# Optimization experiments

Measured on AMD Instinct MI355X. Metric: run time of the kernel, lower is better.

Reference implementation:

```python
import jax, jax.numpy as jnp
import numpy as np

B, S, D, H = 4, 2048, 1024, 16
HS = D // H  # head_size = 64


def setup_inputs() -> dict:
    key = jax.random.key(0)
    ks = jax.random.split(key, 6)
    scale = 0.02
    return {
        "token_embeddings": jax.random.normal(ks[0], (B, S, D), dtype=jnp.float32),
        # per-head projection weights, stacked: [H, D, HS] (x @ W per head)
        "Wq": jax.random.normal(ks[1], (H, D, HS), dtype=jnp.float32) * scale,
        "Wk": jax.random.normal(ks[2], (H, D, HS), dtype=jnp.float32) * scale,
        "Wv": jax.random.normal(ks[3], (H, D, HS), dtype=jnp.float32) * scale,
        # output projection (Linear with bias): y = x @ Wo + bo
        "Wo": jax.random.normal(ks[4], (D, D), dtype=jnp.float32) * scale,
        "bo": jax.random.normal(ks[5], (D,), dtype=jnp.float32) * scale,
    }


def reference(token_embeddings, Wq, Wk, Wv, Wo, bo):
    # Per-head projections, batched over heads: [B,H,S,HS]
    q = jnp.einsum("bsd,hde->bhse", token_embeddings, Wq)
    k = jnp.einsum("bsd,hde->bhse", token_embeddings, Wk)
    v = jnp.einsum("bsd,hde->bhse", token_embeddings, Wv)
    scale = HS ** -0.5
    scores = jnp.einsum("bhqe,bhke->bhqk", q, k) * scale  # [B,H,S,S]
    causal = jnp.tril(jnp.ones((S, S), dtype=bool))
    scores = jnp.where(causal, scores, -jnp.inf)
    weights = jax.nn.softmax(scores, axis=-1)
    # dropout in eval mode -> identity
    out = jnp.einsum("bhqk,bhke->bhqe", weights, v)  # [B,H,S,HS]
    # concat heads -> [B,S,D] (head order matches torch.cat over heads)
    out = out.transpose(0, 2, 1, 3).reshape(B, S, D)
    return out @ Wo + bo
```

## Files before the change

kernel.cpp:

```cpp
#include <hip/hip_runtime.h>


typedef __bf16 bf16;
typedef bf16 bf16x8 __attribute__((ext_vector_type(8)));
typedef bf16 bf16x4 __attribute__((ext_vector_type(4)));
typedef float f32x4 __attribute__((ext_vector_type(4)));

__device__ __forceinline__ void gload16(const void* gsrc, void* ldst) {
  __builtin_amdgcn_global_load_lds(
      (const __attribute__((address_space(1))) unsigned int*)gsrc,
      (__attribute__((address_space(3))) unsigned int*)ldst, 16, 0, 0);
}

__device__ __forceinline__ f32x4 mfma16(bf16x8 a, bf16x8 b, f32x4 c) {
  return __builtin_amdgcn_mfma_f32_16x16x32_bf16(a, b, c, 0, 0, 0);
}

__global__ __launch_bounds__(256) void pack_x_kernel(const float* __restrict__ x,
                                                     bf16* __restrict__ xb) {
  int i = (blockIdx.x * 256 + threadIdx.x) * 4;
  float4 v = *(const float4*)(x + i);
  bf16x4 o;
  o[0] = (bf16)v.x; o[1] = (bf16)v.y; o[2] = (bf16)v.z; o[3] = (bf16)v.w;
  *(bf16x4*)(xb + i) = o;
}

__global__ __launch_bounds__(256) void pack_wqkv_kernel(const float* __restrict__ Wq,
                                                        const float* __restrict__ Wk,
                                                        const float* __restrict__ Wv,
                                                        bf16* __restrict__ WT) {
  int idx = blockIdx.x * 256 + threadIdx.x;
  int n = idx >> 10, k = idx & 1023;
  int sel = n >> 10, nn = n & 1023;
  const float* W = (sel == 0) ? Wq : (sel == 1 ? Wk : Wv);
  int h = nn >> 6, e = nn & 63;
  WT[(size_t)n * 1024 + k] = (bf16)W[h * 65536 + k * 64 + e];
}

__global__ __launch_bounds__(256) void pack_wo_kernel(const float* __restrict__ Wo,
                                                      bf16* __restrict__ WoT) {
  int idx = blockIdx.x * 256 + threadIdx.x;
  int n = idx >> 10, k = idx & 1023;
  WoT[idx] = (bf16)Wo[k * 1024 + n];
}

template <bool F32OUT>
__global__ __launch_bounds__(256, 2) void gemm4_kernel(const bf16* __restrict__ A,
                                                       const bf16* __restrict__ BT,
                                                       bf16* __restrict__ Cb,
                                                       float* __restrict__ Cf,
                                                       const float* __restrict__ bias,
                                                       int N, int K) {
  __shared__ bf16 As[2][128 * 64];
  __shared__ bf16 Bs[2][128 * 64];
  const int tid = threadIdx.x, lane = tid & 63, wave = tid >> 6;
  const int g = lane >> 4, c = lane & 15;
  const int wr = wave >> 1, wc = wave & 1;
  const int bid = blockIdx.x;
  const int xcd = bid & 7, local = bid >> 3;
  const int m0 = (xcd * 8 + (local & 7)) * 128;
  const int n0 = (local >> 3) * 128;

  const int schunk = (lane & 7) ^ (lane >> 3);

#define STAGE4(T, S)                                                      \
  do {                                                                    \
    _Pragma("unroll") for (int j = 0; j < 4; ++j) {                       \
      const int r = wave * 32 + j * 8 + (lane >> 3);                      \
      const int ldso = wave * 4096 + j * 1024 + lane * 16;                \
      gload16(A + (size_t)(m0 + r) * K + (T)*64 + schunk * 8,             \
              (char*)&As[S][0] + ldso);                                   \
      gload16(BT + (size_t)(n0 + r) * K + (T)*64 + schunk * 8,            \
              (char*)&Bs[S][0] + ldso);                                   \
    }                                                                     \
  } while (0)

  f32x4 acc[4][4] = {};
  const int nt = K >> 6;
  STAGE4(0, 0);
  asm volatile("s_waitcnt vmcnt(0)" ::: "memory");
  __builtin_amdgcn_sched_barrier(0);
  __builtin_amdgcn_s_barrier();
  __builtin_amdgcn_sched_barrier(0);

#pragma unroll 1
  for (int t = 0; t < nt; ++t) {
    const int s = t & 1;
    if (t + 1 < nt) STAGE4(t + 1, s ^ 1);
    bf16x8 af[4][2], bfr[4][2];
#pragma unroll
    for (int m = 0; m < 4; ++m) {
      const int row = wr * 64 + m * 16 + c;
#pragma unroll
      for (int kk = 0; kk < 2; ++kk)
        af[m][kk] = *(const bf16x8*)((const char*)&As[s][0] + row * 128 +
                                     (((kk * 4 + g) ^ (row & 7)) << 4));
    }
#pragma unroll
    for (int n = 0; n < 4; ++n) {
      const int row = wc * 64 + n * 16 + c;
#pragma unroll
      for (int kk = 0; kk < 2; ++kk)
        bfr[n][kk] = *(const bf16x8*)((const char*)&Bs[s][0] + row * 128 +
                                      (((kk * 4 + g) ^ (row & 7)) << 4));
    }
    __builtin_amdgcn_s_setprio(1);
#pragma unroll
    for (int kk = 0; kk < 2; ++kk)
#pragma unroll
      for (int m = 0; m < 4; ++m)
#pragma unroll
        for (int n = 0; n < 4; ++n)
          acc[m][n] = mfma16(af[m][kk], bfr[n][kk], acc[m][n]);
    __builtin_amdgcn_s_setprio(0);
    if (t + 1 < nt) {
      asm volatile("s_waitcnt vmcnt(0)" ::: "memory");
      __builtin_amdgcn_sched_barrier(0);
      __builtin_amdgcn_s_barrier();
      __builtin_amdgcn_sched_barrier(0);
    }
  }
#undef STAGE4
#pragma unroll
  for (int m = 0; m < 4; ++m)
#pragma unroll
    for (int n = 0; n < 4; ++n)
#pragma unroll
      for (int i = 0; i < 4; ++i) {
        int row = m0 + wr * 64 + m * 16 + g * 4 + i;
        int col = n0 + wc * 64 + n * 16 + c;
        if (F32OUT)
          Cf[(size_t)row * N + col] = acc[m][n][i] + bias[col];
        else
          Cb[(size_t)row * N + col] = (bf16)acc[m][n][i];
      }
}

__global__ __launch_bounds__(256) void transpose_v_kernel(const bf16* __restrict__ qkv,
                                                          bf16* __restrict__ vt) {
  __shared__ bf16 tl[64][72];
  const int tid = threadIdx.x;
  const int st = blockIdx.x, bh = blockIdx.y;
  const int b = bh >> 4, h = bh & 15;
#pragma unroll
  for (int it = 0; it < 2; ++it) {
    int idx = it * 256 + tid;
    int sl = idx >> 3, ch = idx & 7;
    bf16x8 v = *(const bf16x8*)(qkv + (size_t)(b * 2048 + st * 64 + sl) * 3072 + 2048 + h * 64 + ch * 8);
    *(bf16x8*)&tl[sl][ch * 8] = v;
  }
  __syncthreads();
#pragma unroll
  for (int it = 0; it < 2; ++it) {
    int idx = it * 256 + tid;
    int d = idx >> 3, ch = idx & 7;
    const int blk = ch >> 2, g = ch & 3;
    bf16x8 o;
#pragma unroll
    for (int j = 0; j < 8; ++j) {
      int loc = (j < 4) ? (4 * g + j) : (16 + 4 * g + (j - 4));
      o[j] = tl[blk * 32 + loc][d];
    }
    *(bf16x8*)(vt + ((size_t)bh * 64 + d) * 2048 + st * 64 + ch * 8) = o;
  }
}

__global__ __launch_bounds__(512, 4) void attn_kernel(const bf16* __restrict__ qkv,
                                                      const bf16* __restrict__ vt,
                                                      bf16* __restrict__ attn_out) {
  __shared__ bf16 Ks[2][128 * 64];
  __shared__ bf16 Vs[2][64 * 128];
  const int tid = threadIdx.x, lane = tid & 63, wave = tid >> 6;
  const int g = lane >> 4, c = lane & 15;
  const int bid = blockIdx.x;
  const int xcd = bid & 7;
  const int x = (bid >> 3) & 7;
  const int bh = (bid >> 6) * 8 + xcd;
  const int b = bh >> 4, h = bh & 15;
  const float SCL = 0.125f * 1.4426950408889634f;

  bf16x8 ones;
#pragma unroll
  for (int j = 0; j < 8; ++j) ones[j] = (bf16)1.0f;

#define STAGE(KT, BUF)                                                                    \
  do {                                                                                    \
    _Pragma("unroll") for (int t2 = 0; t2 < 2; ++t2) {                                    \
      int o = t2 * 8192 + wave * 1024 + lane * 16;                          \
      int rK = o >> 7, chK = (((o & 127) >> 4) ^ (rK & 7));                               \
      gload16((const char*)qkv +                                                          \
                  ((size_t)(b * 2048 + (KT)*128 + rK) * 3072 + 1024 + h * 64) * 2 +       \
                  (chK << 4),                                                             \
              (char*)Ks[BUF] + o);                                                        \
      int rV = o >> 8, chV = (((o & 255) >> 4) ^ (rV & 7));                               \
      gload16((const char*)vt + (((size_t)bh * 64 + rV) * 2048 + (KT)*128) * 2 +          \
                  (chV << 4),                                                             \
              (char*)Vs[BUF] + o);                                                        \
    }                                                                                     \
  } while (0)

#pragma unroll 1
  for (int ph = 0; ph < 2; ++ph) {
    const int qt = ph ? (15 - x) : x;
    const int qlow = qt * 128 + wave * 16;

    bf16x8 qf[2];
#pragma unroll
    for (int kk = 0; kk < 2; ++kk) {
      size_t row = (size_t)(b * 2048 + qlow + c);
      qf[kk] = *(const bf16x8*)(qkv + row * 3072 + h * 64 + kk * 32 + g * 8);
    }

    f32x4 oacc[4] = {};
    f32x4 lacc = {};
    float mrun = -3.0e38f;

    const int nkt = qt + 1;
    STAGE(0, 0);
    for (int kt = 0; kt < nkt; ++kt) {
      const int cur = kt & 1;
      if (kt + 1 < nkt) {
        STAGE(kt + 1, cur ^ 1);
        asm volatile("s_waitcnt vmcnt(4)" ::: "memory");
      } else {
        asm volatile("s_waitcnt vmcnt(0)" ::: "memory");
      }
      __builtin_amdgcn_sched_barrier(0);
      __builtin_amdgcn_s_barrier();
      __builtin_amdgcn_sched_barrier(0);
      f32x4 sc[8] = {};
      __builtin_amdgcn_s_setprio(1);
#pragma unroll
      for (int n = 0; n < 8; ++n) {
        int key = n * 16 + c;
#pragma unroll
        for (int kk = 0; kk < 2; ++kk) {
          bf16x8 kf = *(const bf16x8*)((const char*)Ks[cur] + key * 128 +
                                       (((kk * 4 + g) ^ (key & 7)) << 4));
          sc[n] = mfma16(kf, qf[kk], sc[n]);
        }
      }
      __builtin_amdgcn_s_setprio(0);
      const int q = qlow + c;
      if (kt == qt) {
#pragma unroll
        for (int n = 0; n < 8; ++n)
#pragma unroll
          for (int i = 0; i < 4; ++i)
            sc[n][i] = ((kt * 128 + n * 16 + 4 * g + i) <= q) ? sc[n][i] : -3.0e38f;
      }
      float vmax;
      {
        float a[8];
#pragma unroll
        for (int n = 0; n < 8; ++n)
          a[n] = fmaxf(fmaxf(sc[n][0], sc[n][1]), fmaxf(sc[n][2], sc[n][3]));
        float b0 = fmaxf(a[0], a[1]), b1 = fmaxf(a[2], a[3]);
        float b2 = fmaxf(a[4], a[5]), b3 = fmaxf(a[6], a[7]);
        vmax = fmaxf(fmaxf(b0, b1), fmaxf(b2, b3));
      }
      vmax = fmaxf(vmax, __shfl_xor(vmax, 16));
      vmax = fmaxf(vmax, __shfl_xor(vmax, 32));
      const float mx = vmax * SCL;
      if (!__all(mx <= mrun + 8.0f)) {
        const float mnew = fmaxf(mrun, mx);
        const float fs = __builtin_amdgcn_exp2f(mrun - mnew);
        mrun = mnew;
#pragma unroll
        for (int i = 0; i < 4; ++i) {
          float fsb = __shfl(fs, ((lane >> 4) << 2) + i);
          lacc[i] *= fsb;
#pragma unroll
          for (int dn = 0; dn < 4; ++dn) oacc[dn][i] *= fsb;
        }
      }
#pragma unroll
      for (int n = 0; n < 8; ++n)
#pragma unroll
        for (int i = 0; i < 4; ++i)
          sc[n][i] = __builtin_amdgcn_exp2f(fmaf(sc[n][i], SCL, -mrun));
      bf16x8 pa[4];
#pragma unroll
      for (int kss = 0; kss < 4; ++kss) {
        bf16x8 t;
#pragma unroll
        for (int j = 0; j < 4; ++j) t[j] = (bf16)sc[2 * kss][j];
#pragma unroll
        for (int j = 0; j < 4; ++j) t[4 + j] = (bf16)sc[2 * kss + 1][j];
        pa[kss] = t;
      }
      __builtin_amdgcn_s_setprio(1);
#pragma unroll
      for (int kss = 0; kss < 4; ++kss) {
        lacc = mfma16(pa[kss], ones, lacc);
#pragma unroll
        for (int dn = 0; dn < 4; ++dn) {
          const int d = dn * 16 + c;
          bf16x8 vb = *(const bf16x8*)((const char*)Vs[cur] + d * 256 +
                                       (((kss * 4 + g) ^ (d & 7)) << 4));
          oacc[dn] = mfma16(pa[kss], vb, oacc[dn]);
        }
      }
      __builtin_amdgcn_s_setprio(0);
      __builtin_amdgcn_sched_barrier(0);
      __builtin_amdgcn_s_barrier();
      __builtin_amdgcn_sched_barrier(0);
    }
#pragma unroll
    for (int i = 0; i < 4; ++i) {
      float inv = __builtin_amdgcn_rcpf(lacc[i]);
      size_t row = (size_t)(b * 2048 + qlow + 4 * g + i);
#pragma unroll
      for (int dn = 0; dn < 4; ++dn)
        attn_out[row * 1024 + h * 64 + dn * 16 + c] = (bf16)(oacc[dn][i] * inv);
    }
  }
#undef STAGE
}

extern "C" void kernel_launch(void* const* d_in, const int* in_sizes, int n_in,
                              void* d_out, int out_size, void* d_ws, size_t ws_size,
                              hipStream_t stream) {
  const float* x  = (const float*)d_in[0];
  const float* Wq = (const float*)d_in[1];
  const float* Wk = (const float*)d_in[2];
  const float* Wv = (const float*)d_in[3];
  const float* Wo = (const float*)d_in[4];
  const float* bo = (const float*)d_in[5];
  float* out = (float*)d_out;
  char* ws = (char*)d_ws;

  bf16* Xb    = (bf16*)(ws);
  bf16* WqkvT = (bf16*)(ws + 16777216);
  bf16* WoT   = (bf16*)(ws + 23068672);
  bf16* QKV   = (bf16*)(ws + 25165824);
  bf16* VT    = (bf16*)(ws + 75497472);
  bf16* AttnO = (bf16*)(ws + 92274688);

  pack_x_kernel<<<8192, 256, 0, stream>>>(x, Xb);
  pack_wqkv_kernel<<<12288, 256, 0, stream>>>(Wq, Wk, Wv, WqkvT);
  pack_wo_kernel<<<4096, 256, 0, stream>>>(Wo, WoT);
  gemm4_kernel<false><<<1536, 256, 0, stream>>>(Xb, WqkvT, QKV, nullptr, nullptr,
                                                3072, 1024);
  transpose_v_kernel<<<dim3(32, 64), 256, 0, stream>>>(QKV, VT);
  attn_kernel<<<512, 512, 0, stream>>>(QKV, VT, AttnO);
  gemm4_kernel<true><<<512, 256, 0, stream>>>(AttnO, WoT, nullptr, out, bo,
                                              1024, 1024);
}
```

Before: 172.5 us.

## Use 256x128 GEMM tiles with 512 threads and triple-buffered LDS prefetch

```diff
diff --git a/kernel.cpp b/kernel.cpp
--- a/kernel.cpp
+++ b/kernel.cpp
@@ -45,48 +45,54 @@
 }
 
 template <bool F32OUT>
-__global__ __launch_bounds__(256, 2) void gemm4_kernel(const bf16* __restrict__ A,
+__global__ __launch_bounds__(512, 2) void gemm5_kernel(const bf16* __restrict__ A,
                                                        const bf16* __restrict__ BT,
                                                        bf16* __restrict__ Cb,
                                                        float* __restrict__ Cf,
                                                        const float* __restrict__ bias,
                                                        int N, int K) {
-  __shared__ bf16 As[2][128 * 64];
-  __shared__ bf16 Bs[2][128 * 64];
+  __shared__ bf16 As[3][256 * 64];
+  __shared__ bf16 Bs[3][128 * 64];
   const int tid = threadIdx.x, lane = tid & 63, wave = tid >> 6;
   const int g = lane >> 4, c = lane & 15;
   const int wr = wave >> 1, wc = wave & 1;
   const int bid = blockIdx.x;
   const int xcd = bid & 7, local = bid >> 3;
-  const int m0 = (xcd * 8 + (local & 7)) * 128;
-  const int n0 = (local >> 3) * 128;
-
-  const int schunk = (lane & 7) ^ (lane >> 3);
-
-#define STAGE4(T, S)                                                      \
-  do {                                                                    \
-    _Pragma("unroll") for (int j = 0; j < 4; ++j) {                       \
-      const int r = wave * 32 + j * 8 + (lane >> 3);                      \
-      const int ldso = wave * 4096 + j * 1024 + lane * 16;                \
-      gload16(A + (size_t)(m0 + r) * K + (T)*64 + schunk * 8,             \
-              (char*)&As[S][0] + ldso);                                   \
-      gload16(BT + (size_t)(n0 + r) * K + (T)*64 + schunk * 8,            \
-              (char*)&Bs[S][0] + ldso);                                   \
-    }                                                                     \
+  const int m0 = (xcd * 4 + (local & 3)) * 256;
+  const int n0 = (local >> 2) * 128;
+
+  const int rsub = tid >> 3;
+  const int sch = (tid & 7) ^ (rsub & 7);
+
+#define STAGE5(T, S)                                                        \
+  do {                                                                      \
+    _Pragma("unroll") for (int j = 0; j < 4; ++j) {                         \
+      gload16(A + (size_t)(m0 + j * 64 + rsub) * K + (T)*64 + sch * 8,      \
+              (char*)&As[S][0] + j * 8192 + tid * 16);                      \
+    }                                                                       \
+    _Pragma("unroll") for (int j = 0; j < 2; ++j) {                         \
+      gload16(BT + (size_t)(n0 + j * 64 + rsub) * K + (T)*64 + sch * 8,     \
+              (char*)&Bs[S][0] + j * 8192 + tid * 16);                      \
+    }                                                                       \
   } while (0)
 
   f32x4 acc[4][4] = {};
   const int nt = K >> 6;
-  STAGE4(0, 0);
-  asm volatile("s_waitcnt vmcnt(0)" ::: "memory");
-  __builtin_amdgcn_sched_barrier(0);
-  __builtin_amdgcn_s_barrier();
-  __builtin_amdgcn_sched_barrier(0);
+  STAGE5(0, 0);
+  STAGE5(1, 1);
 
 #pragma unroll 1
   for (int t = 0; t < nt; ++t) {
-    const int s = t & 1;
-    if (t + 1 < nt) STAGE4(t + 1, s ^ 1);
+    const int s = t % 3;
+    if (t + 1 < nt) {
+      asm volatile("s_waitcnt vmcnt(6)" ::: "memory");
+    } else {
+      asm volatile("s_waitcnt vmcnt(0)" ::: "memory");
+    }
+    __builtin_amdgcn_sched_barrier(0);
+    __builtin_amdgcn_s_barrier();
+    __builtin_amdgcn_sched_barrier(0);
+    if (t + 2 < nt) STAGE5(t + 2, (t + 2) % 3);
     bf16x8 af[4][2], bfr[4][2];
 #pragma unroll
     for (int m = 0; m < 4; ++m) {
@@ -113,14 +119,8 @@
         for (int n = 0; n < 4; ++n)
           acc[m][n] = mfma16(af[m][kk], bfr[n][kk], acc[m][n]);
     __builtin_amdgcn_s_setprio(0);
-    if (t + 1 < nt) {
-      asm volatile("s_waitcnt vmcnt(0)" ::: "memory");
-      __builtin_amdgcn_sched_barrier(0);
-      __builtin_amdgcn_s_barrier();
-      __builtin_amdgcn_sched_barrier(0);
-    }
   }
-#undef STAGE4
+#undef STAGE5
 #pragma unroll
   for (int m = 0; m < 4; ++m)
 #pragma unroll
@@ -340,10 +340,10 @@
   pack_x_kernel<<<8192, 256, 0, stream>>>(x, Xb);
   pack_wqkv_kernel<<<12288, 256, 0, stream>>>(Wq, Wk, Wv, WqkvT);
   pack_wo_kernel<<<4096, 256, 0, stream>>>(Wo, WoT);
-  gemm4_kernel<false><<<1536, 256, 0, stream>>>(Xb, WqkvT, QKV, nullptr, nullptr,
-                                                3072, 1024);
+  gemm5_kernel<false><<<768, 512, 0, stream>>>(Xb, WqkvT, QKV, nullptr, nullptr,
+                                               3072, 1024);
   transpose_v_kernel<<<dim3(32, 64), 256, 0, stream>>>(QKV, VT);
   attn_kernel<<<512, 512, 0, stream>>>(QKV, VT, AttnO);
-  gemm4_kernel<true><<<512, 256, 0, stream>>>(AttnO, WoT, nullptr, out, bo,
+  gemm5_kernel<true><<<256, 512, 0, stream>>>(AttnO, WoT, nullptr, out, bo,
                                               1024, 1024);
 }
```

Measured after the change: 186.3 us. +8.0%, slower.

## Merge pack kernels into one grid-stride launch and restructure attention loop barriers

Applied to the files above, without the earlier changes.

```diff
diff --git a/kernel.cpp b/kernel.cpp
--- a/kernel.cpp
+++ b/kernel.cpp
@@ -16,32 +16,33 @@
   return __builtin_amdgcn_mfma_f32_16x16x32_bf16(a, b, c, 0, 0, 0);
 }
 
-__global__ __launch_bounds__(256) void pack_x_kernel(const float* __restrict__ x,
-                                                     bf16* __restrict__ xb) {
-  int i = (blockIdx.x * 256 + threadIdx.x) * 4;
-  float4 v = *(const float4*)(x + i);
-  bf16x4 o;
-  o[0] = (bf16)v.x; o[1] = (bf16)v.y; o[2] = (bf16)v.z; o[3] = (bf16)v.w;
-  *(bf16x4*)(xb + i) = o;
-}
-
-__global__ __launch_bounds__(256) void pack_wqkv_kernel(const float* __restrict__ Wq,
-                                                        const float* __restrict__ Wk,
-                                                        const float* __restrict__ Wv,
-                                                        bf16* __restrict__ WT) {
-  int idx = blockIdx.x * 256 + threadIdx.x;
-  int n = idx >> 10, k = idx & 1023;
-  int sel = n >> 10, nn = n & 1023;
-  const float* W = (sel == 0) ? Wq : (sel == 1 ? Wk : Wv);
-  int h = nn >> 6, e = nn & 63;
-  WT[(size_t)n * 1024 + k] = (bf16)W[h * 65536 + k * 64 + e];
-}
-
-__global__ __launch_bounds__(256) void pack_wo_kernel(const float* __restrict__ Wo,
-                                                      bf16* __restrict__ WoT) {
-  int idx = blockIdx.x * 256 + threadIdx.x;
-  int n = idx >> 10, k = idx & 1023;
-  WoT[idx] = (bf16)Wo[k * 1024 + n];
+__global__ __launch_bounds__(256) void pack_all_kernel(const float* __restrict__ x,
+                                                       const float* __restrict__ Wq,
+                                                       const float* __restrict__ Wk,
+                                                       const float* __restrict__ Wv,
+                                                       const float* __restrict__ Wo,
+                                                       bf16* __restrict__ xb,
+                                                       bf16* __restrict__ WT,
+                                                       bf16* __restrict__ WoT) {
+  const int stride = gridDim.x * 256;
+  const int t0 = blockIdx.x * 256 + threadIdx.x;
+  for (int i = t0; i < 2097152; i += stride) {
+    float4 v = *(const float4*)(x + (size_t)i * 4);
+    bf16x4 o;
+    o[0] = (bf16)v.x; o[1] = (bf16)v.y; o[2] = (bf16)v.z; o[3] = (bf16)v.w;
+    *(bf16x4*)(xb + (size_t)i * 4) = o;
+  }
+  for (int idx = t0; idx < 3145728; idx += stride) {
+    int n = idx >> 10, k = idx & 1023;
+    int sel = n >> 10, nn = n & 1023;
+    const float* W = (sel == 0) ? Wq : (sel == 1 ? Wk : Wv);
+    int h = nn >> 6, e = nn & 63;
+    WT[(size_t)n * 1024 + k] = (bf16)W[h * 65536 + k * 64 + e];
+  }
+  for (int idx = t0; idx < 1048576; idx += stride) {
+    int n = idx >> 10, k = idx & 1023;
+    WoT[idx] = (bf16)Wo[k * 1024 + n];
+  }
 }
 
 template <bool F32OUT>
@@ -216,18 +217,16 @@
     float mrun = -3.0e38f;
 
     const int nkt = qt + 1;
+    __builtin_amdgcn_s_barrier();
+    __builtin_amdgcn_sched_barrier(0);
     STAGE(0, 0);
+    asm volatile("s_waitcnt vmcnt(0)" ::: "memory");
+    __builtin_amdgcn_sched_barrier(0);
+    __builtin_amdgcn_s_barrier();
+    __builtin_amdgcn_sched_barrier(0);
     for (int kt = 0; kt < nkt; ++kt) {
       const int cur = kt & 1;
-      if (kt + 1 < nkt) {
-        STAGE(kt + 1, cur ^ 1);
-        asm volatile("s_waitcnt vmcnt(4)" ::: "memory");
-      } else {
-        asm volatile("s_waitcnt vmcnt(0)" ::: "memory");
-      }
-      __builtin_amdgcn_sched_barrier(0);
-      __builtin_amdgcn_s_barrier();
-      __builtin_amdgcn_sched_barrier(0);
+      if (kt + 1 < nkt) STAGE(kt + 1, cur ^ 1);
       f32x4 sc[8] = {};
       __builtin_amdgcn_s_setprio(1);
 #pragma unroll
@@ -302,9 +301,12 @@
         }
       }
       __builtin_amdgcn_s_setprio(0);
-      __builtin_amdgcn_sched_barrier(0);
-      __builtin_amdgcn_s_barrier();
-      __builtin_amdgcn_sched_barrier(0);
+      if (kt + 1 < nkt) {
+        asm volatile("s_waitcnt vmcnt(0)" ::: "memory");
+        __builtin_amdgcn_sched_barrier(0);
+        __builtin_amdgcn_s_barrier();
+        __builtin_amdgcn_sched_barrier(0);
+      }
     }
 #pragma unroll
     for (int i = 0; i < 4; ++i) {
@@ -337,9 +339,7 @@
   bf16* VT    = (bf16*)(ws + 75497472);
   bf16* AttnO = (bf16*)(ws + 92274688);
 
-  pack_x_kernel<<<8192, 256, 0, stream>>>(x, Xb);
-  pack_wqkv_kernel<<<12288, 256, 0, stream>>>(Wq, Wk, Wv, WqkvT);
-  pack_wo_kernel<<<4096, 256, 0, stream>>>(Wo, WoT);
+  pack_all_kernel<<<2048, 256, 0, stream>>>(x, Wq, Wk, Wv, Wo, Xb, WqkvT, WoT);
   gemm4_kernel<false><<<1536, 256, 0, stream>>>(Xb, WqkvT, QKV, nullptr, nullptr,
                                                 3072, 1024);
   transpose_v_kernel<<<dim3(32, 64), 256, 0, stream>>>(QKV, VT);
```

Measured after the change: 167.5 us. 2.9% less time.
